# Optimization experiments

Measured on AMD Instinct MI355X. Metric: run time of the kernel, lower is better.

Reference implementation:

```python
import jax, jax.numpy as jnp
import numpy as np

B, S, H = 1, 2048, 2048
NH, NKV, DH = 8, 1, 256
ROPE_THETA = 10000.0
SCALE = DH ** -0.5
NEG = -1e9


def setup_inputs() -> dict:
    key = jax.random.key(0)
    k1, k2, k3, k4, k5 = jax.random.split(key, 5)
    x = jax.random.normal(k1, (B, S, H), dtype=jnp.float32)
    position_ids = jnp.broadcast_to(jnp.arange(S, dtype=jnp.int32)[None, :], (B, S))
    causal = jnp.tril(jnp.ones((S, S), dtype=bool))
    attention_mask = jnp.where(causal, 0.0, NEG).astype(jnp.float32)[None, None]  # [1,1,S,S]
    std = 0.02
    w_q = jax.random.normal(k2, (H, NH * DH), dtype=jnp.float32) * std
    w_k = jax.random.normal(k3, (H, NKV * DH), dtype=jnp.float32) * std
    w_v = jax.random.normal(k4, (H, NKV * DH), dtype=jnp.float32) * std
    w_o = jax.random.normal(k5, (NH * DH, H), dtype=jnp.float32) * std
    return {"x": x, "position_ids": position_ids, "attention_mask": attention_mask,
            "w_q": w_q, "w_k": w_k, "w_v": w_v, "w_o": w_o}


def _rope_cos_sin(position_ids):
    # inv_freq: [DH/2]
    inv_freq = 1.0 / (ROPE_THETA ** (jnp.arange(0, DH, 2, dtype=jnp.float32) / DH))
    freqs = position_ids.astype(jnp.float32)[:, :, None] * inv_freq[None, None, :]  # [B,S,DH/2]
    emb = jnp.concatenate([freqs, freqs], axis=-1)  # [B,S,DH]
    return jnp.cos(emb), jnp.sin(emb)


def _rotate_half(t):
    t1, t2 = jnp.split(t, 2, axis=-1)
    return jnp.concatenate([-t2, t1], axis=-1)


def reference(x, position_ids, attention_mask, w_q, w_k, w_v, w_o):
    b, s, _ = x.shape
    g = NH // NKV  # kv group size
    q = (x @ w_q).reshape(b, s, NH, DH).transpose(0, 2, 1, 3)   # [b,nh,s,d]
    k = (x @ w_k).reshape(b, s, NKV, DH).transpose(0, 2, 1, 3)  # [b,nkv,s,d]
    v = (x @ w_v).reshape(b, s, NKV, DH).transpose(0, 2, 1, 3)
    cos, sin = _rope_cos_sin(position_ids)
    cos, sin = cos[:, None], sin[:, None]  # broadcast over heads
    q = q * cos + _rotate_half(q) * sin
    k = k * cos + _rotate_half(k) * sin
    # GQA: view q as [b,nkv,g,s,d]; equivalent to repeat_kv without materializing
    qg = q.reshape(b, NKV, g, s, DH)
    scores = jnp.einsum('bkgid,bkjd->bkgij', qg, k) * SCALE      # [b,nkv,g,s,s]
    scores = scores + attention_mask[:, :, None, :, :]
    attn = jax.nn.softmax(scores.astype(jnp.float32), axis=-1).astype(q.dtype)
    out = jnp.einsum('bkgij,bkjd->bkgid', attn, v)               # [b,nkv,g,s,d]
    out = out.reshape(b, NH, s, DH).transpose(0, 2, 1, 3).reshape(b, s, NH * DH)
    out = out @ w_o
    return out, attn.reshape(b, NH, s, s)
```

## Files before the change

kernel.cpp:

```cpp
#include <hip/hip_runtime.h>
#include <hip/hip_bf16.h>
#include <hip/hip_fp16.h>

typedef float f32x4 __attribute__((ext_vector_type(4)));
typedef _Float16 half8 __attribute__((ext_vector_type(8)));
typedef unsigned short u16;

#define DEVI __device__ __forceinline__

DEVI void async_cp16(void* lds, const void* g) {
  __builtin_amdgcn_global_load_lds(
      (const __attribute__((address_space(1))) void*)g,
      (__attribute__((address_space(3))) void*)lds,
      16, 0, 0);
}

DEVI u16 f2h(float x) {
  union { _Float16 h; u16 u; } v;
  v.h = (_Float16)x;
  return v.u;
}

__global__ __launch_bounds__(256)
void k_prep(const float* __restrict__ x, const float* __restrict__ wq,
            const float* __restrict__ wk, const float* __restrict__ wv,
            const float* __restrict__ wo,
            u16* __restrict__ xb, u16* __restrict__ wqkvT, u16* __restrict__ woT) {
  int bx = blockIdx.x;
  if (bx >= 72) {
    size_t base = ((size_t)(bx - 72) * 32 + blockIdx.y) * 2048 + threadIdx.x * 8;
    float4 v0 = *(const float4*)(x + base);
    float4 v1 = *(const float4*)(x + base + 4);
    ushort4 o0, o1;
    o0.x = f2h(v0.x); o0.y = f2h(v0.y); o0.z = f2h(v0.z); o0.w = f2h(v0.w);
    o1.x = f2h(v1.x); o1.y = f2h(v1.y); o1.z = f2h(v1.z); o1.w = f2h(v1.w);
    *(ushort4*)(xb + base) = o0;
    *(ushort4*)(xb + base + 4) = o1;
    return;
  }
  __shared__ u16 tile[64][65];
  const float* in; int ldin, rowoff, cx; u16* out;
  if (bx < 32)      { in = wq; ldin = 2048; out = wqkvT; rowoff = 0;    cx = bx; }
  else if (bx < 36) { in = wk; ldin = 256;  out = wqkvT; rowoff = 2048; cx = bx - 32; }
  else if (bx < 40) { in = wv; ldin = 256;  out = wqkvT; rowoff = 2304; cx = bx - 36; }
  else              { in = wo; ldin = 2048; out = woT;   rowoff = 0;    cx = bx - 40; }
  int r0 = blockIdx.y * 64, c0 = cx * 64;
  int tx = threadIdx.x & 63, ty = threadIdx.x >> 6;
  for (int rr = ty; rr < 64; rr += 4)
    tile[rr][tx] = f2h(in[(size_t)(r0 + rr) * ldin + (c0 + tx)]);
  __syncthreads();
  for (int rr = ty; rr < 64; rr += 4)
    out[(size_t)(c0 + rr + rowoff) * 2048 + (r0 + tx)] = tile[tx][rr];
}

__global__ __launch_bounds__(256)
void k_transpose2(const float* __restrict__ in0, const float* __restrict__ in1,
                  int ldin, u16* __restrict__ out, int ldout) {
  __shared__ u16 tile[64][65];
  int r0 = blockIdx.y * 64, c0 = blockIdx.x * 64;
  int tx = threadIdx.x & 63, ty = threadIdx.x >> 6;
  for (int rr = ty; rr < 64; rr += 4) {
    size_t idx = (size_t)(r0 + rr) * ldin + (c0 + tx);
    tile[rr][tx] = f2h(in0[idx] + in1[idx]);
  }
  __syncthreads();
  for (int rr = ty; rr < 64; rr += 4)
    out[(size_t)(c0 + rr) * ldout + (r0 + tx)] = tile[tx][rr];
}

__global__ __launch_bounds__(256)
void k_gemm128(const u16* __restrict__ A, int lda,
               const u16* __restrict__ B, int ldb,
               float* __restrict__ C0, float* __restrict__ C1,
               int ldc, int nmt, int Kloc) {
  const int bx = blockIdx.x;
  const int mt = bx % nmt, split = bx / nmt;
  float* __restrict__ C = split ? C1 : C0;
  const int i0 = mt * 128, j0 = blockIdx.y * 128;
  const size_t koff = (size_t)split * Kloc;

  __shared__ __align__(16) u16 As[2][128 * 32];
  __shared__ __align__(16) u16 Bs[2][128 * 32];
  const int tid = threadIdx.x;
  const int wave = tid >> 6, lane = tid & 63;
  const int wm = (wave >> 1) * 64, wn = (wave & 1) * 64;
  const int quad = lane >> 4, r = lane & 15;

  f32x4 acc[4][4] = {};

  const int ar = tid >> 2, ac = (tid & 3) * 8;
  const u16* ag0 = A + (size_t)(i0 + ar) * lda + ac + koff;
  const u16* ag1 = ag0 + (size_t)64 * lda;
  const u16* bg0 = B + (size_t)(j0 + ar) * ldb + ac + koff;
  const u16* bg1 = bg0 + (size_t)64 * ldb;
  const int l0 = tid * 8, l1 = (tid + 256) * 8;

  async_cp16(As[0] + l0, ag0); async_cp16(As[0] + l1, ag1);
  async_cp16(Bs[0] + l0, bg0); async_cp16(Bs[0] + l1, bg1);
  ag0 += 32; ag1 += 32; bg0 += 32; bg1 += 32;
  __syncthreads();

  const int nk = Kloc >> 5;
  for (int kt = 0; kt < nk; kt += 2) {
#pragma unroll
    for (int half = 0; half < 2; half++) {
      int cur = half, nxt = half ^ 1;
      if (kt + half + 1 < nk) {
        async_cp16(As[nxt] + l0, ag0); async_cp16(As[nxt] + l1, ag1);
        async_cp16(Bs[nxt] + l0, bg0); async_cp16(Bs[nxt] + l1, bg1);
        ag0 += 32; ag1 += 32; bg0 += 32; bg1 += 32;
      }
      half8 af[4], bf[4];
#pragma unroll
      for (int t = 0; t < 4; t++) af[t] = *(const half8*)(As[cur] + (wm + t * 16 + r) * 32 + quad * 8);
#pragma unroll
      for (int t = 0; t < 4; t++) bf[t] = *(const half8*)(Bs[cur] + (wn + t * 16 + r) * 32 + quad * 8);
#pragma unroll
      for (int ta = 0; ta < 4; ta++)
#pragma unroll
        for (int tb = 0; tb < 4; tb++)
          acc[ta][tb] = __builtin_amdgcn_mfma_f32_16x16x32_f16(af[ta], bf[tb], acc[ta][tb], 0, 0, 0);
      __syncthreads();
    }
  }
#pragma unroll
  for (int ta = 0; ta < 4; ta++) {
#pragma unroll
    for (int tb = 0; tb < 4; tb++) {
      int row = i0 + wm + ta * 16 + quad * 4;
      int col = j0 + wn + tb * 16 + r;
      float* cp = C + (size_t)row * ldc + col;
#pragma unroll
      for (int v = 0; v < 4; v++) cp[(size_t)v * ldc] = acc[ta][tb][v];
    }
  }
}

__global__ __launch_bounds__(256)
void k_add(float* __restrict__ dst, const float* __restrict__ src) {
  size_t idx = (size_t)blockIdx.x * 256 + threadIdx.x;
  float4 a = ((const float4*)dst)[idx];
  float4 b = ((const float4*)src)[idx];
  a.x += b.x; a.y += b.y; a.z += b.z; a.w += b.w;
  ((float4*)dst)[idx] = a;
}

__global__ __launch_bounds__(256)
void k_rope(const float* __restrict__ qkv0, const float* __restrict__ qkv1,
            const int* __restrict__ pos,
            u16* __restrict__ qh, u16* __restrict__ kh) {
  int idx = blockIdx.x * 256 + threadIdx.x;
  const int TOTAL_Q = 2048 * 1024;
  int s, i;
  size_t off;
  u16* dst;
  if (idx < TOTAL_Q) {
    s = idx >> 10;
    int hi = idx & 1023;
    int hd = hi >> 7;
    i = hi & 127;
    off = (size_t)s * 2560 + hd * 256;
    dst = qh + (size_t)s * 2048 + hd * 256;
  } else {
    int t = idx - TOTAL_Q;
    s = t >> 7;
    i = t & 127;
    off = (size_t)s * 2560 + 2048;
    dst = kh + (size_t)s * 256;
  }
  float p = (float)pos[s];
  float freq = __expf((float)i * (-9.210340371976184f / 128.0f)) * p;
  float sn, cs;
  sincosf(freq, &sn, &cs);
  float a = qkv0[off + i] + qkv1[off + i];
  float b = qkv0[off + i + 128] + qkv1[off + i + 128];
  dst[i]       = f2h(a * cs - b * sn);
  dst[i + 128] = f2h(b * cs + a * sn);
}

__global__ __launch_bounds__(256)
void k_scores(const u16* __restrict__ qh, const u16* __restrict__ kh,
              float* __restrict__ attn, float* __restrict__ lsum) {
  const int i0 = blockIdx.y * 128, j0 = blockIdx.x * 128;
  const int h = blockIdx.z;
  const int tid = threadIdx.x;
  float* outb = attn + ((size_t)h << 22);
  if (j0 > i0) {
    float4 z = {0.f, 0.f, 0.f, 0.f};
    int row = tid >> 5, col4 = (tid & 31) * 4;
    for (int s = 0; s < 16; s++)
      *(float4*)(outb + (size_t)(i0 + s * 8 + row) * 2048 + j0 + col4) = z;
    return;
  }
  const u16* A = qh + h * 256;
  __shared__ __align__(16) u16 As[2][128 * 32];
  __shared__ __align__(16) u16 Bs[2][128 * 32];
  __shared__ float psum[128];
  const int wave = tid >> 6, lane = tid & 63;
  const int wm = (wave >> 1) * 64, wn = (wave & 1) * 64;
  const int quad = lane >> 4, r = lane & 15;

  f32x4 acc[4][4] = {};

  const int ar = tid >> 2, ac = (tid & 3) * 8;
  const u16* ag0 = A + (size_t)(i0 + ar) * 2048 + ac;
  const u16* ag1 = ag0 + (size_t)64 * 2048;
  const u16* bg0 = kh + (size_t)(j0 + ar) * 256 + ac;
  const u16* bg1 = bg0 + (size_t)64 * 256;
  const int l0 = tid * 8, l1 = (tid + 256) * 8;

  async_cp16(As[0] + l0, ag0); async_cp16(As[0] + l1, ag1);
  async_cp16(Bs[0] + l0, bg0); async_cp16(Bs[0] + l1, bg1);
  ag0 += 32; ag1 += 32; bg0 += 32; bg1 += 32;
  __syncthreads();

  for (int kt = 0; kt < 8; kt += 2) {
#pragma unroll
    for (int half = 0; half < 2; half++) {
      int cur = half, nxt = half ^ 1;
      if (kt + half + 1 < 8) {
        async_cp16(As[nxt] + l0, ag0); async_cp16(As[nxt] + l1, ag1);
        async_cp16(Bs[nxt] + l0, bg0); async_cp16(Bs[nxt] + l1, bg1);
        ag0 += 32; ag1 += 32; bg0 += 32; bg1 += 32;
      }
      half8 af[4], bf[4];
#pragma unroll
      for (int t = 0; t < 4; t++) af[t] = *(const half8*)(As[cur] + (wm + t * 16 + r) * 32 + quad * 8);
#pragma unroll
      for (int t = 0; t < 4; t++) bf[t] = *(const half8*)(Bs[cur] + (wn + t * 16 + r) * 32 + quad * 8);
#pragma unroll
      for (int ta = 0; ta < 4; ta++)
#pragma unroll
        for (int tb = 0; tb < 4; tb++)
          acc[ta][tb] = __builtin_amdgcn_mfma_f32_16x16x32_f16(af[ta], bf[tb], acc[ta][tb], 0, 0, 0);
      __syncthreads();
    }
  }

  if (tid < 128) psum[tid] = 0.f;
  __syncthreads();
#pragma unroll
  for (int ta = 0; ta < 4; ta++) {
#pragma unroll
    for (int v = 0; v < 4; v++) {
      int row = i0 + wm + ta * 16 + quad * 4 + v;
      float rs = 0.f;
#pragma unroll
      for (int tb = 0; tb < 4; tb++) {
        int col = j0 + wn + tb * 16 + r;
        float val = (col <= row) ? __expf(acc[ta][tb][v] * 0.0625f) : 0.0f;
        outb[(size_t)row * 2048 + col] = val;
        rs += val;
      }
      rs += __shfl_xor(rs, 1); rs += __shfl_xor(rs, 2);
      rs += __shfl_xor(rs, 4); rs += __shfl_xor(rs, 8);
      if (r == 0) atomicAdd(&psum[wm + ta * 16 + quad * 4 + v], rs);
    }
  }
  __syncthreads();
  if (tid < 128)
    lsum[((size_t)h * 2048 + i0 + tid) * 16 + blockIdx.x] = psum[tid];
}

__global__ __launch_bounds__(256)
void k_pv(float* __restrict__ attn, const u16* __restrict__ vT,
          const float* __restrict__ lsum, u16* __restrict__ o) {
  const int h = blockIdx.y;
  const int i0 = blockIdx.x * 32;
  float* Ab = attn + ((size_t)h << 22);
  const int kmax = i0 + 32;
  __shared__ __align__(16) u16 As[32 * 32];
  __shared__ __align__(16) u16 Bs[256 * 32];
  __shared__ float inv_l[32];
  const int tid = threadIdx.x;
  const int wave = tid >> 6, lane = tid & 63;
  const int wn = wave * 64;
  const int quad = lane >> 4, r = lane & 15;

  if (tid < 32) {
    int i = i0 + tid;
    const float* lp = lsum + ((size_t)h * 2048 + i) * 16;
    int nt = (i >> 7) + 1;
    float s = 0.f;
    for (int t = 0; t < nt; t++) s += lp[t];
    inv_l[tid] = 1.0f / s;
  }
  __syncthreads();

  f32x4 acc[2][4] = {};
  const int br = tid >> 2, bc = (tid & 3) * 8;
  const u16* bg = vT + (size_t)br * 2048 + bc;
  const int arr = tid >> 3, ac4 = (tid & 7) * 4;
  float* agp = Ab + (size_t)(i0 + arr) * 2048 + ac4;
  const float ainv = inv_l[arr];

  for (int k0 = 0; k0 < kmax; k0 += 32) {
#pragma unroll
    for (int c = 0; c < 4; c++)
      async_cp16(Bs + tid * 8 + c * 2048, bg + (size_t)(c * 64) * 2048 + k0);
    float4 v = *(const float4*)(agp + k0);
    v.x *= ainv; v.y *= ainv; v.z *= ainv; v.w *= ainv;
    *(float4*)(agp + k0) = v;
    ushort4 w;
    w.x = f2h(v.x); w.y = f2h(v.y); w.z = f2h(v.z); w.w = f2h(v.w);
    *(ushort4*)(As + arr * 32 + ac4) = w;
    __syncthreads();
    half8 af[2], bf[4];
#pragma unroll
    for (int t = 0; t < 2; t++) af[t] = *(const half8*)(As + (t * 16 + r) * 32 + quad * 8);
#pragma unroll
    for (int t = 0; t < 4; t++) bf[t] = *(const half8*)(Bs + (wn + t * 16 + r) * 32 + quad * 8);
#pragma unroll
    for (int ta = 0; ta < 2; ta++)
#pragma unroll
      for (int tb = 0; tb < 4; tb++)
        acc[ta][tb] = __builtin_amdgcn_mfma_f32_16x16x32_f16(af[ta], bf[tb], acc[ta][tb], 0, 0, 0);
    __syncthreads();
  }
#pragma unroll
  for (int ta = 0; ta < 2; ta++) {
    int row = i0 + ta * 16 + quad * 4;
#pragma unroll
    for (int tb = 0; tb < 4; tb++) {
      int col = h * 256 + wn + tb * 16 + r;
#pragma unroll
      for (int v = 0; v < 4; v++)
        o[(size_t)(row + v) * 2048 + col] = f2h(acc[ta][tb][v]);
    }
  }
}

extern "C" void kernel_launch(void* const* d_in, const int* in_sizes, int n_in,
                              void* d_out, int out_size, void* d_ws, size_t ws_size,
                              hipStream_t stream) {
  const float* x   = (const float*)d_in[0];
  const int*   pos = (const int*)d_in[1];
  const float* w_q = (const float*)d_in[3];
  const float* w_k = (const float*)d_in[4];
  const float* w_v = (const float*)d_in[5];
  const float* w_o = (const float*)d_in[6];

  float* out  = (float*)d_out;
  float* attn = out + (size_t)2048 * 2048;

  char* ws = (char*)d_ws;
  float* qkv0  = (float*)ws;
  u16*   xb    = (u16*)(ws + (size_t)2048 * 2560 * 4);
  u16*   wqkvT = xb + (size_t)2048 * 2048;
  u16*   woT   = wqkvT + (size_t)2560 * 2048;
  u16*   qh    = woT + (size_t)2048 * 2048;
  u16*   kh    = qh + (size_t)2048 * 2048;
  u16*   vT    = kh + (size_t)2048 * 256;
  u16*   ob    = vT + (size_t)256 * 2048;
  float* lsum  = (float*)(ob + (size_t)2048 * 2048);

  float* qkv1  = attn;
  float* outp1 = (float*)xb;

  k_prep<<<dim3(136, 32), 256, 0, stream>>>(x, w_q, w_k, w_v, w_o, xb, wqkvT, woT);

  k_gemm128<<<dim3(32, 20), 256, 0, stream>>>(xb, 2048, wqkvT, 2048, qkv0, qkv1, 2560, 16, 1024);

  k_rope<<<(2048 * 1024 + 2048 * 128) / 256, 256, 0, stream>>>(qkv0, qkv1, pos, qh, kh);
  k_transpose2<<<dim3(4, 32), 256, 0, stream>>>(qkv0 + 2304, qkv1 + 2304, 2560, vT, 2048);

  k_scores<<<dim3(16, 16, 8), 256, 0, stream>>>(qh, kh, attn, lsum);
  k_pv<<<dim3(64, 8), 256, 0, stream>>>(attn, vT, lsum, ob);

  k_gemm128<<<dim3(32, 16), 256, 0, stream>>>(ob, 2048, woT, 2048, out, outp1, 2048, 16, 1024);
  k_add<<<4096, 256, 0, stream>>>(out, outp1);
}
```

Before: 385.7 us.

## Replace 128x128 GEMM with 256x256 tile, 4-stage async pipeline and swizzled LDS

Replaces the projection GEMM kernel with a 512-thread version that computes 256x256 output tiles. It uses a 4-buffer async global-to-LDS pipeline with explicit vmcnt waits, an XOR-swizzled LDS layout to avoid bank conflicts, and an XCD-aware block index mapping. Barriers and s_setprio are interleaved so prefetch overlaps the MFMA work. Larger tiles raise data reuse, but they also cut the number of blocks to 160 and 128, which risks leaving CUs idle and raises register pressure.

```diff
diff --git a/kernel.cpp b/kernel.cpp
--- a/kernel.cpp
+++ b/kernel.cpp
@@ -68,72 +68,127 @@
     out[(size_t)(c0 + rr) * ldout + (r0 + tx)] = tile[tx][rr];
 }
 
-__global__ __launch_bounds__(256)
-void k_gemm128(const u16* __restrict__ A, int lda,
+__global__ __launch_bounds__(512, 2)
+void k_gemm256(const u16* __restrict__ A, int lda,
                const u16* __restrict__ B, int ldb,
                float* __restrict__ C0, float* __restrict__ C1,
-               int ldc, int nmt, int Kloc) {
-  const int bx = blockIdx.x;
-  const int mt = bx % nmt, split = bx / nmt;
+               int ldc, int nN, int Kloc) {
+  const int id = blockIdx.x;
+  const int xcd = id & 7, t = id >> 3;
+  const int by = t % nN;
+  const int ms = xcd + 8 * (t / nN);
+  const int mt = ms & 7, split = ms >> 3;
   float* __restrict__ C = split ? C1 : C0;
-  const int i0 = mt * 128, j0 = blockIdx.y * 128;
+  const int i0 = mt * 256, j0 = by * 256;
   const size_t koff = (size_t)split * Kloc;
 
-  __shared__ __align__(16) u16 As[2][128 * 32];
-  __shared__ __align__(16) u16 Bs[2][128 * 32];
+  __shared__ __align__(16) u16 AB[4][16384];
   const int tid = threadIdx.x;
   const int wave = tid >> 6, lane = tid & 63;
-  const int wm = (wave >> 1) * 64, wn = (wave & 1) * 64;
+  const int wm = (wave >> 2) * 128, wn = (wave & 3) * 64;
   const int quad = lane >> 4, r = lane & 15;
 
-  f32x4 acc[4][4] = {};
-
-  const int ar = tid >> 2, ac = (tid & 3) * 8;
-  const u16* ag0 = A + (size_t)(i0 + ar) * lda + ac + koff;
-  const u16* ag1 = ag0 + (size_t)64 * lda;
-  const u16* bg0 = B + (size_t)(j0 + ar) * ldb + ac + koff;
-  const u16* bg1 = bg0 + (size_t)64 * ldb;
-  const int l0 = tid * 8, l1 = (tid + 256) * 8;
-
-  async_cp16(As[0] + l0, ag0); async_cp16(As[0] + l1, ag1);
-  async_cp16(Bs[0] + l0, bg0); async_cp16(Bs[0] + l1, bg1);
-  ag0 += 32; ag1 += 32; bg0 += 32; bg1 += 32;
-  __syncthreads();
+  f32x4 acc[8][4] = {};
+
+  const int P0 = tid * 16;
+  const int P1 = tid * 16 + 8192;
+  const int L0 = P0 ^ (((P0 >> 7) & 7) << 4);
+  const int row0 = L0 >> 6, col0 = (L0 & 63) >> 1;
+  const u16* srcA0 = A + (size_t)(i0 + row0) * lda + koff + col0;
+  const u16* srcA1 = A + (size_t)(i0 + row0 + 128) * lda + koff + col0;
+  const u16* srcB0 = B + (size_t)(j0 + row0) * ldb + koff + col0;
+  const u16* srcB1 = B + (size_t)(j0 + row0 + 128) * ldb + koff + col0;
+
+  int aoff[2][4], boff[2][2];
+#pragma unroll
+  for (int mi = 0; mi < 2; mi++)
+#pragma unroll
+    for (int m = 0; m < 4; m++) {
+      int row = wm + mi * 64 + m * 16 + r;
+      int L = row * 64 + quad * 16;
+      aoff[mi][m] = L ^ (((row >> 1) & 7) << 4);
+    }
+#pragma unroll
+  for (int ni = 0; ni < 2; ni++)
+#pragma unroll
+    for (int n = 0; n < 2; n++) {
+      int row = wn + ni * 32 + n * 16 + r;
+      int L = row * 64 + quad * 16;
+      boff[ni][n] = L ^ (((row >> 1) & 7) << 4);
+    }
 
   const int nk = Kloc >> 5;
-  for (int kt = 0; kt < nk; kt += 2) {
-#pragma unroll
-    for (int half = 0; half < 2; half++) {
-      int cur = half, nxt = half ^ 1;
-      if (kt + half + 1 < nk) {
-        async_cp16(As[nxt] + l0, ag0); async_cp16(As[nxt] + l1, ag1);
-        async_cp16(Bs[nxt] + l0, bg0); async_cp16(Bs[nxt] + l1, bg1);
-        ag0 += 32; ag1 += 32; bg0 += 32; bg1 += 32;
+
+  for (int p = 0; p < 3; p++) {
+    char* sA = (char*)AB[p];
+    char* sB = (char*)AB[p] + 16384;
+    async_cp16(sA + P0, srcA0); async_cp16(sA + P1, srcA1);
+    async_cp16(sB + P0, srcB0); async_cp16(sB + P1, srcB1);
+    srcA0 += 32; srcA1 += 32; srcB0 += 32; srcB1 += 32;
+  }
+
+  half8 af[4], bf[2][2];
+  for (int kt = 0; kt < nk; kt++) {
+    if (kt < nk - 2)       asm volatile("s_waitcnt vmcnt(8)" ::: "memory");
+    else if (kt == nk - 2) asm volatile("s_waitcnt vmcnt(4)" ::: "memory");
+    else                   asm volatile("s_waitcnt vmcnt(0)" ::: "memory");
+    __builtin_amdgcn_s_barrier();
+    __builtin_amdgcn_sched_barrier(0);
+
+    const char* rA = (const char*)AB[kt & 3];
+    const char* rB = (const char*)AB[kt & 3] + 16384;
+    const bool pf = (kt + 3 < nk);
+    char* wA = (char*)AB[(kt + 3) & 3];
+    char* wB = (char*)AB[(kt + 3) & 3] + 16384;
+
+#pragma unroll
+    for (int q = 0; q < 4; q++) {
+      const int mi = q >> 1, ni = q & 1;
+      if (ni == 0) {
+#pragma unroll
+        for (int m = 0; m < 4; m++) af[m] = *(const half8*)(rA + aoff[mi][m]);
       }
-      half8 af[4], bf[4];
-#pragma unroll
-      for (int t = 0; t < 4; t++) af[t] = *(const half8*)(As[cur] + (wm + t * 16 + r) * 32 + quad * 8);
-#pragma unroll
-      for (int t = 0; t < 4; t++) bf[t] = *(const half8*)(Bs[cur] + (wn + t * 16 + r) * 32 + quad * 8);
-#pragma unroll
-      for (int ta = 0; ta < 4; ta++)
-#pragma unroll
-        for (int tb = 0; tb < 4; tb++)
-          acc[ta][tb] = __builtin_amdgcn_mfma_f32_16x16x32_f16(af[ta], bf[tb], acc[ta][tb], 0, 0, 0);
-      __syncthreads();
-    }
-  }
-#pragma unroll
-  for (int ta = 0; ta < 4; ta++) {
-#pragma unroll
-    for (int tb = 0; tb < 4; tb++) {
-      int row = i0 + wm + ta * 16 + quad * 4;
-      int col = j0 + wn + tb * 16 + r;
-      float* cp = C + (size_t)row * ldc + col;
-#pragma unroll
-      for (int v = 0; v < 4; v++) cp[(size_t)v * ldc] = acc[ta][tb][v];
-    }
-  }
+      if (mi == 0) {
+#pragma unroll
+        for (int n = 0; n < 2; n++) bf[ni][n] = *(const half8*)(rB + boff[ni][n]);
+      }
+      if (pf) {
+        if (q == 0) async_cp16(wA + P0, srcA0);
+        if (q == 1) async_cp16(wA + P1, srcA1);
+        if (q == 2) async_cp16(wB + P0, srcB0);
+        if (q == 3) async_cp16(wB + P1, srcB1);
+      }
+      __builtin_amdgcn_s_barrier();
+      asm volatile("s_waitcnt lgkmcnt(0)" ::: "memory");
+      __builtin_amdgcn_sched_barrier(0);
+      __builtin_amdgcn_s_setprio(1);
+#pragma unroll
+      for (int m = 0; m < 4; m++)
+#pragma unroll
+        for (int n = 0; n < 2; n++)
+          acc[mi * 4 + m][ni * 2 + n] = __builtin_amdgcn_mfma_f32_16x16x32_f16(
+              af[m], bf[ni][n], acc[mi * 4 + m][ni * 2 + n], 0, 0, 0);
+      __builtin_amdgcn_s_setprio(0);
+      __builtin_amdgcn_s_barrier();
+    }
+    if (pf) { srcA0 += 32; srcA1 += 32; srcB0 += 32; srcB1 += 32; }
+  }
+
+#pragma unroll
+  for (int mi = 0; mi < 2; mi++)
+#pragma unroll
+    for (int m = 0; m < 4; m++) {
+      int row = i0 + wm + mi * 64 + m * 16 + quad * 4;
+#pragma unroll
+      for (int ni = 0; ni < 2; ni++)
+#pragma unroll
+        for (int n = 0; n < 2; n++) {
+          int col = j0 + wn + ni * 32 + n * 16 + r;
+          float* cp = C + (size_t)row * ldc + col;
+#pragma unroll
+          for (int v = 0; v < 4; v++) cp[(size_t)v * ldc] = acc[mi * 4 + m][ni * 2 + n][v];
+        }
+    }
 }
 
 __global__ __launch_bounds__(256)
@@ -359,7 +414,7 @@
 
   k_prep<<<dim3(136, 32), 256, 0, stream>>>(x, w_q, w_k, w_v, w_o, xb, wqkvT, woT);
 
-  k_gemm128<<<dim3(32, 20), 256, 0, stream>>>(xb, 2048, wqkvT, 2048, qkv0, qkv1, 2560, 16, 1024);
+  k_gemm256<<<dim3(160), 512, 0, stream>>>(xb, 2048, wqkvT, 2048, qkv0, qkv1, 2560, 10, 1024);
 
   k_rope<<<(2048 * 1024 + 2048 * 128) / 256, 256, 0, stream>>>(qkv0, qkv1, pos, qh, kh);
   k_transpose2<<<dim3(4, 32), 256, 0, stream>>>(qkv0 + 2304, qkv1 + 2304, 2560, vT, 2048);
@@ -367,6 +422,6 @@
   k_scores<<<dim3(16, 16, 8), 256, 0, stream>>>(qh, kh, attn, lsum);
   k_pv<<<dim3(64, 8), 256, 0, stream>>>(attn, vT, lsum, ob);
 
-  k_gemm128<<<dim3(32, 16), 256, 0, stream>>>(ob, 2048, woT, 2048, out, outp1, 2048, 16, 1024);
+  k_gemm256<<<dim3(128), 512, 0, stream>>>(ob, 2048, woT, 2048, out, outp1, 2048, 8, 1024);
   k_add<<<4096, 256, 0, stream>>>(out, outp1);
 }
```

New measurement: 380.6 us. No clear change (-1.3%).
